# Kernel optimization log

Measured on AMD Instinct MI355X. Metric: run time of the kernel, lower is better.

Reference implementation:

```python
import jax, jax.numpy as jnp
import numpy as np

DIM = 1024
H_HEADS = 16


def setup_inputs() -> dict:
    key = jax.random.key(0)
    ks = jax.random.split(key, 12)
    h, w = 48, 80
    hw = h * w
    n_frames, n_sel = 11, 384
    wscale = 1.0 / np.sqrt(DIM).astype(np.float32)
    return {
        "feats_cur": jax.random.normal(ks[0], (1, DIM, h, w), jnp.float32),
        "ps": jax.random.normal(ks[1], (1, DIM, h, w), jnp.float32),
        "feats_ref": jax.random.normal(ks[2], (n_frames, DIM, h, w), jnp.float32),
        "ext_mem": jax.random.normal(ks[3], (24000, DIM), jnp.float32),
        "glob_cache": jax.random.normal(ks[4], (4000, DIM), jnp.float32),
        "Wq": jax.random.normal(ks[5], (DIM, DIM), jnp.float32) * wscale,
        "Wk": jax.random.normal(ks[6], (DIM, DIM), jnp.float32) * wscale,
        "Wv": jax.random.normal(ks[7], (DIM, DIM), jnp.float32) * wscale,
        "Wo": jax.random.normal(ks[8], (DIM, DIM), jnp.float32) * wscale,
        "ref_sel_idx": jax.random.randint(ks[9], (n_frames, n_sel), 0, hw, jnp.int32),
        "mem_idx": jax.random.randint(ks[10], (2000,), 0, 24000, jnp.int32),
        "glob_idx": jax.random.randint(ks[11], (2000,), 0, 4000, jnp.int32),
    }


def reference(feats_cur, ps, feats_ref, ext_mem, glob_cache, Wq, Wk, Wv, Wo,
              ref_sel_idx, mem_idx, glob_idx):
    b, dim, h, w = feats_cur.shape
    hw = h * w
    # current-frame pixels with positional encoding -> queries [hw, dim]
    q_in = (feats_cur + ps)[0].reshape(dim, hw).T
    # reference frames + ps -> [F, hw, dim], sparse randperm-style subsample via precomputed indices
    ref = (feats_ref + ps).reshape(-1, dim, hw).transpose(0, 2, 1)
    sel = jnp.take_along_axis(ref, ref_sel_idx[:, :, None], axis=1).reshape(-1, dim)
    # concat with subsampled external memory and global cache pixels
    k_in = jnp.concatenate([sel, ext_mem[mem_idx], glob_cache[glob_idx]], axis=0)  # [Nk, dim]
    dh = dim // H_HEADS
    scale = 1.0 / np.sqrt(dh).astype(np.float32)
    q = (q_in @ Wq).reshape(hw, H_HEADS, dh)
    k = (k_in @ Wk).reshape(-1, H_HEADS, dh)
    v = (k_in @ Wv).reshape(-1, H_HEADS, dh)
    logits = jnp.einsum('qhd,khd->hqk', q, k) * scale  # [H, hw, Nk]
    attn = jax.nn.softmax(logits, axis=-1)
    ctx = jnp.einsum('hqk,khd->qhd', attn, v).reshape(hw, dim)
    out = q_in + ctx @ Wo  # residual, like MEGA relation module
    # back to [1, dim, h, w] as in update_lm_pixel_with_transpose
    return out.T.reshape(1, dim, h, w)
```

## Files before the change

kernel.cpp:

```cpp
#include <hip/hip_runtime.h>

using u16 = unsigned short;
using bf16x8 = __attribute__((ext_vector_type(8))) short;
using f32x4  = __attribute__((ext_vector_type(4))) float;

#define DIM   1024
#define HW    3840
#define NSEL  4224
#define NK    8224
#define NKPAD 8320
#define NH    16
#define KVB   64
#define THR   50.0f

typedef __attribute__((address_space(1))) const unsigned GU;
typedef __attribute__((address_space(3))) unsigned LU;

__device__ __forceinline__ u16 f2bf(float x) {
    unsigned u = __float_as_uint(x);
    return (u16)((u + 0x7FFFu + ((u >> 16) & 1u)) >> 16);
}

__device__ __forceinline__ float exp2fast(float x) {
    return __builtin_amdgcn_exp2f(x);
}

__global__ void prep_kernel(const float* __restrict__ Wq, const float* __restrict__ Wk,
                            const float* __restrict__ Wv, const float* __restrict__ Wo,
                            const float* __restrict__ fc, const float* __restrict__ ps,
                            const float* __restrict__ fr, const float* __restrict__ em,
                            const float* __restrict__ gc, const int* __restrict__ sel,
                            const int* __restrict__ midx, const int* __restrict__ gidx,
                            u16* __restrict__ WT, u16* __restrict__ qin, u16* __restrict__ kin) {
    const int b = blockIdx.x;
    const int tid = threadIdx.x;
    if (b < 4096) {
        const int zz = b >> 10, yy = (b >> 5) & 31, xx = b & 31;
        const float* src = zz == 0 ? Wq : zz == 1 ? Wk : zz == 2 ? Wv : Wo;
        u16* dst = WT + (size_t)zz * DIM * DIM;
        __shared__ float t[32][33];
        const int n0 = xx * 32, k0 = yy * 32;
        const int tx = tid & 31, ty = tid >> 5;
#pragma unroll
        for (int j = 0; j < 4; ++j)
            t[ty + 8 * j][tx] = src[(size_t)(k0 + ty + 8 * j) * DIM + n0 + tx];
        __syncthreads();
#pragma unroll
        for (int j = 0; j < 4; ++j)
            dst[(size_t)(n0 + ty + 8 * j) * DIM + k0 + tx] = f2bf(t[tx][ty + 8 * j]);
    } else if (b < 7936) {
        const int bb = b - 4096;
        const int xx = bb % 120, yy = bb / 120;
        __shared__ float t[32][33];
        const int p0 = xx * 32, d0 = yy * 32;
        const int tx = tid & 31, ty = tid >> 5;
#pragma unroll
        for (int j = 0; j < 4; ++j) {
            int d = d0 + ty + 8 * j;
            t[ty + 8 * j][tx] = fc[(size_t)d * HW + p0 + tx] + ps[(size_t)d * HW + p0 + tx];
        }
        __syncthreads();
#pragma unroll
        for (int j = 0; j < 4; ++j)
            qin[(size_t)(p0 + ty + 8 * j) * DIM + d0 + tx] = f2bf(t[tx][ty + 8 * j]);
    } else {
        const int row = b - 7936;
        u16* dst = kin + (size_t)row * DIM;
        const int t = tid;
        if (row < NSEL) {
            const int f = row / 384;
            const int idx = sel[row];
            const float* base = fr + (size_t)f * DIM * HW + idx;
#pragma unroll
            for (int j = 0; j < 4; ++j) {
                int d = t + 256 * j;
                dst[d] = f2bf(base[(size_t)d * HW] + ps[(size_t)d * HW + idx]);
            }
        } else if (row < NSEL + 2000) {
            const float* src = em + (size_t)midx[row - NSEL] * DIM;
#pragma unroll
            for (int j = 0; j < 4; ++j) { int d = t + 256 * j; dst[d] = f2bf(src[d]); }
        } else if (row < NK) {
            const float* src = gc + (size_t)gidx[row - (NSEL + 2000)] * DIM;
#pragma unroll
            for (int j = 0; j < 4; ++j) { int d = t + 256 * j; dst[d] = f2bf(src[d]); }
        } else {
#pragma unroll
            for (int j = 0; j < 4; ++j) dst[t + 256 * j] = 0;
        }
    }
}

__device__ __forceinline__ void gemm_bt_body(const u16* __restrict__ A,
                                             const u16* __restrict__ B,
                                             void* __restrict__ Cout,
                                             const float* __restrict__ r1,
                                             const float* __restrict__ r2,
                                             int ldc, int mode, float scale,
                                             int bx, int by) {
    __shared__ __align__(16) u16 As[128 * 64];
    __shared__ __align__(16) u16 Bs[128 * 64];
    const int tid = threadIdx.x;
    const int l = tid & 63;
    const int wv = tid >> 6;
    const int wr = (wv >> 1) * 64, wc = (wv & 1) * 64;
    const int g = l >> 4, lo = l & 15;
    const size_t bm = (size_t)by * 128, bn = (size_t)bx * 128;
    const f32x4 fzero = {0.f, 0.f, 0.f, 0.f};

    f32x4 acc[4][4];
#pragma unroll
    for (int i = 0; i < 4; ++i)
#pragma unroll
        for (int j = 0; j < 4; ++j) acc[i][j] = fzero;

#define GSTAGE(KT)                                                                              \
    {                                                                                           \
        const int k0_ = (KT) * 64;                                                              \
        _Pragma("unroll") for (int q = 0; q < 4; ++q) {                                         \
            const int idx = q * 256 + tid;                                                      \
            const int row = idx >> 3, c8 = idx & 7;                                             \
            const int scol = (c8 ^ (row & 7)) * 8;                                              \
            const int dbase = q * 2048 + wv * 512;                                              \
            __builtin_amdgcn_global_load_lds((GU*)(A + (bm + row) * DIM + k0_ + scol),          \
                                             (LU*)&As[dbase], 16, 0, 0);                        \
            __builtin_amdgcn_global_load_lds((GU*)(B + (bn + row) * DIM + k0_ + scol),          \
                                             (LU*)&Bs[dbase], 16, 0, 0);                        \
        }                                                                                       \
    }

#define GCOMPUTE()                                                                              \
    {                                                                                           \
        _Pragma("unroll") for (int ks = 0; ks < 2; ++ks) {                                      \
            bf16x8 af[4], bfv[4];                                                               \
            _Pragma("unroll") for (int mi = 0; mi < 4; ++mi) {                                  \
                const int row = wr + mi * 16 + lo;                                              \
                const int sw = (ks * 4 + g) ^ (row & 7);                                        \
                af[mi] = *(const bf16x8*)(&As[row * 64 + sw * 8]);                              \
            }                                                                                   \
            _Pragma("unroll") for (int ni = 0; ni < 4; ++ni) {                                  \
                const int row = wc + ni * 16 + lo;                                              \
                const int sw = (ks * 4 + g) ^ (row & 7);                                        \
                bfv[ni] = *(const bf16x8*)(&Bs[row * 64 + sw * 8]);                             \
            }                                                                                   \
            _Pragma("unroll") for (int mi = 0; mi < 4; ++mi)                                    \
                _Pragma("unroll") for (int ni = 0; ni < 4; ++ni)                                \
                    acc[mi][ni] = __builtin_amdgcn_mfma_f32_16x16x32_bf16(af[mi], bfv[ni], acc[mi][ni], 0, 0, 0); \
        }                                                                                       \
    }

#pragma unroll 1
    for (int kt = 0; kt < 16; ++kt) {
        GSTAGE(kt)
        asm volatile("s_waitcnt vmcnt(0)" ::: "memory");
        __syncthreads();
        GCOMPUTE()
        __syncthreads();
    }
#undef GCOMPUTE
#undef GSTAGE

    if (mode == 0) {
        u16* C = (u16*)Cout;
#pragma unroll
        for (int mi = 0; mi < 4; ++mi)
#pragma unroll
            for (int ni = 0; ni < 4; ++ni)
#pragma unroll
                for (int r = 0; r < 4; ++r) {
                    size_t m = bm + wr + mi * 16 + g * 4 + r;
                    size_t n = bn + wc + ni * 16 + lo;
                    C[m * (size_t)ldc + n] = f2bf(acc[mi][ni][r] * scale);
                }
    } else if (mode == 2) {
        u16* C = (u16*)Cout;
#pragma unroll
        for (int mi = 0; mi < 4; ++mi)
#pragma unroll
            for (int ni = 0; ni < 4; ++ni)
#pragma unroll
                for (int r = 0; r < 4; ++r) {
                    size_t m = bm + wr + mi * 16 + g * 4 + r;
                    size_t n = bn + wc + ni * 16 + lo;
                    size_t o = (n >> 6) * ((size_t)NKPAD * 64) + m * 64 + (n & 63);
                    C[o] = f2bf(acc[mi][ni][r] * scale);
                }
    } else {
        float* C = (float*)Cout;
#pragma unroll
        for (int mi = 0; mi < 4; ++mi)
#pragma unroll
            for (int ni = 0; ni < 4; ++ni)
#pragma unroll
                for (int r = 0; r < 4; ++r) {
                    size_t m = bm + wr + mi * 16 + g * 4 + r;
                    size_t n = bn + wc + ni * 16 + lo;
                    size_t o = m * (size_t)ldc + n;
                    C[o] = acc[mi][ni][r] + r1[o] + r2[o];
                }
    }
}

__global__ __launch_bounds__(256, 3) void proj_kernel(const u16* __restrict__ qin,
                                                      const u16* __restrict__ kin,
                                                      const u16* __restrict__ WT,
                                                      u16* __restrict__ Qp,
                                                      u16* __restrict__ Kp,
                                                      u16* __restrict__ Vt) {
    const int b = blockIdx.x;
    if (b < 240) {
        gemm_bt_body(qin, WT, Qp, nullptr, nullptr, 1024, 0, 0.18033688f, b % 8, b / 8);
    } else if (b < 760) {
        const int bb = b - 240;
        gemm_bt_body(kin, WT + 1048576, Kp, nullptr, nullptr, 1024, 2, 1.0f, bb % 8, bb / 8);
    } else {
        const int bb = b - 760;
        gemm_bt_body(WT + 2097152, kin, Vt, nullptr, nullptr, NKPAD, 0, 1.0f, bb % 65, bb / 65);
    }
}

__global__ __launch_bounds__(256, 3) void outproj_kernel(const u16* __restrict__ WTo,
                                                         const u16* __restrict__ ctx,
                                                         float* __restrict__ out,
                                                         const float* __restrict__ fc,
                                                         const float* __restrict__ ps) {
    gemm_bt_body(WTo, ctx, out, fc, ps, HW, 1, 1.0f, blockIdx.x, blockIdx.y);
}

__global__ __launch_bounds__(256, 3) void attn_kernel(const u16* __restrict__ Q,
                                                      const u16* __restrict__ Kh,
                                                      const u16* __restrict__ Vt,
                                                      u16* __restrict__ ctx) {
    __shared__ __align__(16) u16 Kl[2][4096];
    __shared__ __align__(16) u16 Vl[2][4096];
    __shared__ float invl_s[4][32];
    const int h = blockIdx.x;
    const int tid = threadIdx.x;
    const int l = tid & 63, wv = tid >> 6;
    const int g = l >> 4, lo = l & 15;
    const int hoff = h * 64;
    const int qw = blockIdx.y * 128 + wv * 32;
    const f32x4 fzero = {0.f, 0.f, 0.f, 0.f};
    const int sig = (lo >> 2) * 8 + (lo & 3);

    const u16* Ksrc = Kh + (size_t)h * NKPAD * 64;
    const u16* Vsrc = Vt + (size_t)hoff * NKPAD;

    bf16x8 qa[2][2];
#pragma unroll
    for (int mi = 0; mi < 2; ++mi)
#pragma unroll
        for (int ks = 0; ks < 2; ++ks)
            qa[mi][ks] = *(const bf16x8*)(Q + (size_t)(qw + mi * 16 + lo) * DIM + hoff + ks * 32 + g * 8);

    f32x4 acc[2][4];
#pragma unroll
    for (int mi = 0; mi < 2; ++mi)
#pragma unroll
        for (int ni = 0; ni < 4; ++ni) acc[mi][ni] = fzero;
    float mrow[2] = {-1e30f, -1e30f};
    float lsum[2] = {0.f, 0.f};
    float pmax[2] = {-1e30f, -1e30f};

#define STAGE(BUF, IT)                                                                          \
    {                                                                                           \
        const int kks = (IT) * KVB;                                                             \
        _Pragma("unroll") for (int j = 0; j < 2; ++j) {                                         \
            const int inst = wv * 2 + j;                                                        \
            const int r_ = inst * 8 + (l >> 3);                                                 \
            const int c_ = l & 7;                                                               \
            const int hk_ = ((l >> 3) & 3) | ((inst & 1) << 2);                                 \
            const u16* gK = Ksrc + (size_t)(kks + r_) * 64 + ((c_ ^ hk_) * 8);                  \
            __builtin_amdgcn_global_load_lds((GU*)gK, (LU*)&Kl[BUF][inst * 512], 16, 0, 0);     \
            const u16* gV = Vsrc + (size_t)r_ * NKPAD + kks + ((c_ ^ (r_ & 7)) * 8);            \
            __builtin_amdgcn_global_load_lds((GU*)gV, (LU*)&Vl[BUF][inst * 512], 16, 0, 0);     \
        }                                                                                       \
    }

#define COMPUTE(BUF, NT, NS)                                                                    \
    {                                                                                           \
        f32x4 S[2][4];                                                                          \
        _Pragma("unroll") for (int kp = 0; kp < (NT) / 2; ++kp) {                               \
            bf16x8 kf[2][2];                                                                    \
            _Pragma("unroll") for (int k2 = 0; k2 < 2; ++k2)                                    \
                _Pragma("unroll") for (int ks = 0; ks < 2; ++ks) {                              \
                    const int kt = kp * 2 + k2;                                                 \
                    const int row = (kt >> 1) * 32 + (kt & 1) * 4 + sig;                        \
                    const int hk_ = (row & 3) | (((row >> 3) & 1) << 2);                        \
                    const int ck = (ks * 4 + g) ^ hk_;                                          \
                    kf[k2][ks] = *(const bf16x8*)(&Kl[BUF][row * 64 + ck * 8]);                 \
                }                                                                               \
            _Pragma("unroll") for (int mi = 0; mi < 2; ++mi)                                    \
                _Pragma("unroll") for (int k2 = 0; k2 < 2; ++k2) {                              \
                    f32x4 s_ = __builtin_amdgcn_mfma_f32_16x16x32_bf16(kf[k2][0], qa[mi][0], fzero, 0, 0, 0); \
                    S[mi][kp * 2 + k2] = __builtin_amdgcn_mfma_f32_16x16x32_bf16(kf[k2][1], qa[mi][1], s_, 0, 0, 0); \
                }                                                                               \
        }                                                                                       \
        _Pragma("unroll") for (int mi = 0; mi < 2; ++mi)                                        \
            _Pragma("unroll") for (int kt = 0; kt < (NT); ++kt) {                               \
                f32x4 sv = S[mi][kt];                                                           \
                pmax[mi] = fmaxf(pmax[mi], fmaxf(fmaxf(sv[0], sv[1]), fmaxf(sv[2], sv[3])));    \
            }                                                                                   \
        if (__any(fmaxf(pmax[0] - mrow[0], pmax[1] - mrow[1]) > THR)) {                         \
            _Pragma("unroll") for (int mi = 0; mi < 2; ++mi) {                                  \
                float v = pmax[mi];                                                             \
                v = fmaxf(v, __shfl_xor(v, 16));                                                \
                v = fmaxf(v, __shfl_xor(v, 32));                                                \
                float mn = fmaxf(mrow[mi], v);                                                  \
                float fct = exp2fast(mrow[mi] - mn);                                            \
                mrow[mi] = mn;                                                                  \
                lsum[mi] *= fct;                                                                \
                _Pragma("unroll") for (int r = 0; r < 4; ++r) {                                 \
                    float fr_ = __shfl(fct, g * 4 + r);                                         \
                    _Pragma("unroll") for (int ni = 0; ni < 4; ++ni) acc[mi][ni][r] *= fr_;     \
                }                                                                               \
            }                                                                                   \
        }                                                                                       \
        _Pragma("unroll") for (int s = 0; s < (NS); ++s) {                                      \
            bf16x8 vb[4];                                                                       \
            _Pragma("unroll") for (int ni = 0; ni < 4; ++ni) {                                  \
                const int row = ni * 16 + lo;                                                   \
                const int ck = (s * 4 + g) ^ (row & 7);                                         \
                vb[ni] = *(const bf16x8*)(&Vl[BUF][row * 64 + ck * 8]);                         \
            }                                                                                   \
            _Pragma("unroll") for (int mi = 0; mi < 2; ++mi) {                                  \
                float p0 = exp2fast(S[mi][2 * s][0] - mrow[mi]);                                \
                float p1 = exp2fast(S[mi][2 * s][1] - mrow[mi]);                                \
                float p2 = exp2fast(S[mi][2 * s][2] - mrow[mi]);                                \
                float p3 = exp2fast(S[mi][2 * s][3] - mrow[mi]);                                \
                float p4 = exp2fast(S[mi][2 * s + 1][0] - mrow[mi]);                            \
                float p5 = exp2fast(S[mi][2 * s + 1][1] - mrow[mi]);                            \
                float p6 = exp2fast(S[mi][2 * s + 1][2] - mrow[mi]);                            \
                float p7 = exp2fast(S[mi][2 * s + 1][3] - mrow[mi]);                            \
                lsum[mi] += ((p0 + p1) + (p2 + p3)) + ((p4 + p5) + (p6 + p7));                  \
                union { unsigned u[4]; bf16x8 v; } pu;                                          \
                asm("v_cvt_pk_bf16_f32 %0, %1, %2" : "=v"(pu.u[0]) : "v"(p0), "v"(p1));         \
                asm("v_cvt_pk_bf16_f32 %0, %1, %2" : "=v"(pu.u[1]) : "v"(p2), "v"(p3));         \
                asm("v_cvt_pk_bf16_f32 %0, %1, %2" : "=v"(pu.u[2]) : "v"(p4), "v"(p5));         \
                asm("v_cvt_pk_bf16_f32 %0, %1, %2" : "=v"(pu.u[3]) : "v"(p6), "v"(p7));         \
                _Pragma("unroll") for (int ni = 0; ni < 4; ++ni)                                \
                    acc[mi][ni] = __builtin_amdgcn_mfma_f32_16x16x32_bf16(pu.v, vb[ni], acc[mi][ni], 0, 0, 0); \
            }                                                                                   \
        }                                                                                       \
    }

    STAGE(0, 0)
    asm volatile("s_waitcnt vmcnt(0)" ::: "memory");
    __syncthreads();

#pragma unroll 1
    for (int it = 0; it < 128; it += 2) {
        STAGE(1, it + 1)
        COMPUTE(0, 4, 2)
        asm volatile("s_waitcnt vmcnt(0)" ::: "memory");
        __syncthreads();
        STAGE(0, it + 2)
        COMPUTE(1, 4, 2)
        asm volatile("s_waitcnt vmcnt(0)" ::: "memory");
        __syncthreads();
    }
    COMPUTE(0, 2, 1)
#undef COMPUTE
#undef STAGE

#pragma unroll
    for (int mi = 0; mi < 2; ++mi) {
        float t = lsum[mi];
        t += __shfl_xor(t, 16);
        t += __shfl_xor(t, 32);
        lsum[mi] = t;
    }
    if (l < 16) {
        invl_s[wv][lo] = 1.0f / lsum[0];
        invl_s[wv][16 + lo] = 1.0f / lsum[1];
    }
#pragma unroll
    for (int mi = 0; mi < 2; ++mi)
#pragma unroll
        for (int ni = 0; ni < 4; ++ni)
#pragma unroll
            for (int r = 0; r < 4; ++r) {
                float val = acc[mi][ni][r] * invl_s[wv][mi * 16 + g * 4 + r];
                ctx[(size_t)(qw + mi * 16 + g * 4 + r) * DIM + hoff + ni * 16 + lo] = f2bf(val);
            }
}

extern "C" void kernel_launch(void* const* d_in, const int* in_sizes, int n_in,
                              void* d_out, int out_size, void* d_ws, size_t ws_size,
                              hipStream_t stream) {
    const float* fc  = (const float*)d_in[0];
    const float* ps  = (const float*)d_in[1];
    const float* fr  = (const float*)d_in[2];
    const float* em  = (const float*)d_in[3];
    const float* gc  = (const float*)d_in[4];
    const float* Wq  = (const float*)d_in[5];
    const float* Wk  = (const float*)d_in[6];
    const float* Wv  = (const float*)d_in[7];
    const float* Wo  = (const float*)d_in[8];
    const int* sel   = (const int*)d_in[9];
    const int* midx  = (const int*)d_in[10];
    const int* gidx  = (const int*)d_in[11];

    char* w = (char*)d_ws;
    u16* WT  = (u16*)(w);
    u16* qin = (u16*)(w + 8388608ull);
    u16* kin = (u16*)(w + 16252928ull);
    u16* Qp  = (u16*)(w + 33292288ull);
    u16* Kp  = (u16*)(w + 41156608ull);
    u16* Vt  = (u16*)(w + 58195968ull);
    u16* ctx = (u16*)(w + 75235328ull);
    float* out = (float*)d_out;

    prep_kernel<<<dim3(16256), dim3(256), 0, stream>>>(Wq, Wk, Wv, Wo, fc, ps, fr, em, gc,
                                                       sel, midx, gidx, WT, qin, kin);
    proj_kernel<<<dim3(1280), dim3(256), 0, stream>>>(qin, kin, WT, Qp, Kp, Vt);

    attn_kernel<<<dim3(NH, 30), dim3(256), 0, stream>>>(Qp, Kp, Vt, ctx);

    outproj_kernel<<<dim3(30, 8), dim3(256), 0, stream>>>(WT + 3145728, ctx, out, fc, ps);
}
```

Before: 402.5 us.

## Gather reference-frame pixels via coalesced tile loads instead of strided per-row reads

Replaces the per-selected-row gather, which read each channel with a stride of HW floats, with blocks that each stream a 128-pixel strip of one reference frame into LDS through coalesced float4 loads. Every block finds which selected indices fall inside its strip and writes those rows of kin from the LDS tile. This avoids the uncoalesced scattered reads. In exchange it reads every frame in full (11 frames x 1024 channels x 3840 pixels, plus ps) where it previously read only the selected pixels, and it adds extra syncs and atomics.

```diff
diff --git a/kernel.cpp b/kernel.cpp
--- a/kernel.cpp
+++ b/kernel.cpp
@@ -63,20 +63,56 @@
 #pragma unroll
         for (int j = 0; j < 4; ++j)
             qin[(size_t)(p0 + ty + 8 * j) * DIM + d0 + tx] = f2bf(t[tx][ty + 8 * j]);
+    } else if (b < 8266) {
+        const int fb = b - 7936;
+        const int f = fb / 30, tt = fb % 30;
+        const int px0 = tt * 128;
+        __shared__ float tile[64][129];
+        __shared__ int selS[384];
+        __shared__ int hits[384];
+        __shared__ int cnt;
+        if (tid == 0) cnt = 0;
+        selS[tid] = sel[f * 384 + tid];
+        if (tid < 128) selS[256 + tid] = sel[f * 384 + 256 + tid];
+        __syncthreads();
+        for (int j = tid; j < 384; j += 256) {
+            const int idx = selS[j];
+            if (idx >= px0 && idx < px0 + 128) {
+                const int pos = atomicAdd(&cnt, 1);
+                hits[pos] = (j << 8) | (idx - px0);
+            }
+        }
+        __syncthreads();
+        const int nh = cnt;
+        const int wv = tid >> 6, l = tid & 63;
+        const float* frF = fr + (size_t)f * DIM * HW;
+#pragma unroll 1
+        for (int dc = 0; dc < 16; ++dc) {
+            const int d0 = dc * 64;
+#pragma unroll
+            for (int q = 0; q < 8; ++q) {
+                const int e = q * 256 + tid;
+                const int dd = e >> 5, pp = (e & 31) * 4;
+                const float4 a = *(const float4*)(frF + (size_t)(d0 + dd) * HW + px0 + pp);
+                const float4 c = *(const float4*)(ps + (size_t)(d0 + dd) * HW + px0 + pp);
+                tile[dd][pp + 0] = a.x + c.x;
+                tile[dd][pp + 1] = a.y + c.y;
+                tile[dd][pp + 2] = a.z + c.z;
+                tile[dd][pp + 3] = a.w + c.w;
+            }
+            __syncthreads();
+            for (int hh = wv; hh < nh; hh += 4) {
+                const int e2 = hits[hh];
+                const int j = e2 >> 8, p = e2 & 255;
+                kin[(size_t)(f * 384 + j) * DIM + d0 + l] = f2bf(tile[l][p]);
+            }
+            __syncthreads();
+        }
     } else {
-        const int row = b - 7936;
+        const int row = b - 8266 + NSEL;
         u16* dst = kin + (size_t)row * DIM;
         const int t = tid;
-        if (row < NSEL) {
-            const int f = row / 384;
-            const int idx = sel[row];
-            const float* base = fr + (size_t)f * DIM * HW + idx;
-#pragma unroll
-            for (int j = 0; j < 4; ++j) {
-                int d = t + 256 * j;
-                dst[d] = f2bf(base[(size_t)d * HW] + ps[(size_t)d * HW + idx]);
-            }
-        } else if (row < NSEL + 2000) {
+        if (row < NSEL + 2000) {
             const float* src = em + (size_t)midx[row - NSEL] * DIM;
 #pragma unroll
             for (int j = 0; j < 4; ++j) { int d = t + 256 * j; dst[d] = f2bf(src[d]); }
@@ -411,7 +447,7 @@
     u16* ctx = (u16*)(w + 75235328ull);
     float* out = (float*)d_out;
 
-    prep_kernel<<<dim3(16256), dim3(256), 0, stream>>>(Wq, Wk, Wv, Wo, fc, ps, fr, em, gc,
+    prep_kernel<<<dim3(12362), dim3(256), 0, stream>>>(Wq, Wk, Wv, Wo, fc, ps, fr, em, gc,
                                                        sel, midx, gidx, WT, qin, kin);
     proj_kernel<<<dim3(1280), dim3(256), 0, stream>>>(qin, kin, WT, Qp, Kp, Vt);
 
```

Measured after the change: 342.4 us. 14.9% less time.
